# Kernel tuning notes

Hardware: AMD Instinct MI355X
Metric: run time of the kernel (lower is better)

Reference implementation:

```python
import jax, jax.numpy as jnp
import numpy as np

B, TENC, LIS = 32, 2048, 512
HID, EMB, CLS = 512, 256, 64
KEY, VAL, TDEC = 128, 128, 65


def setup_inputs() -> dict:
    key = jax.random.key(0)
    ks = jax.random.split(key, 32)
    s = 0.02
    p = lambda i, shape: jax.random.normal(ks[i], shape, jnp.float32) * s
    return {
        "listener_output": jax.random.normal(ks[0], (B, TENC, LIS), jnp.float32),
        "outputs_length": jax.random.randint(ks[1], (B,), TENC // 2, TENC + 1, jnp.int32),
        "padded_targets": jax.random.randint(ks[2], (B, TDEC), 0, CLS, jnp.int32),
        "teacher_forcing": 1,
        "embed_table": p(3, (CLS, EMB)),
        "W_ih1": p(4, (4 * HID, EMB + VAL)), "W_hh1": p(5, (4 * HID, HID)),
        "b_ih1": p(6, (4 * HID,)), "b_hh1": p(7, (4 * HID,)),
        "W_ih2": p(8, (4 * HID, HID)), "W_hh2": p(9, (4 * HID, HID)),
        "b_ih2": p(10, (4 * HID,)), "b_hh2": p(11, (4 * HID,)),
        "W_s": p(12, (KEY, HID)), "b_s": p(13, (KEY,)),
        "W_h": p(14, (KEY, LIS)), "b_h": p(15, (KEY,)),
        "W_v": p(16, (VAL, LIS)), "b_v": p(17, (VAL,)),
        "W_c": p(18, (CLS, HID + VAL)), "b_c": p(19, (CLS,)),
        "h1_0": p(20, (B, HID)), "c1_0": p(21, (B, HID)),
        "h2_0": p(22, (B, HID)), "c2_0": p(23, (B, HID)),
    }


def _lstm_cell(x, h, c, Wih, Whh, bih, bhh):
    # torch LSTMCell gate order: input, forget, cell, output
    g = x @ Wih.T + bih + h @ Whh.T + bhh
    i, f, gg, o = jnp.split(g, 4, axis=-1)
    c = jax.nn.sigmoid(f) * c + jax.nn.sigmoid(i) * jnp.tanh(gg)
    h = jax.nn.sigmoid(o) * jnp.tanh(c)
    return h, c


def _speller(listener_output, outputs_length, padded_targets, teacher_forcing,
             embed_table, W_ih1, W_hh1, b_ih1, b_hh1, W_ih2, W_hh2, b_ih2, b_hh2,
             W_s, b_s, W_h, b_h, W_v, b_v, W_c, b_c, h1_0, c1_0, h2_0, c2_0):
    Bv, Tenc, _ = listener_output.shape
    timestep = padded_targets.shape[1] - 1
    # time-validity mask; row 0 is left unmasked, matching the original loops (i != 0)
    valid = jnp.arange(Tenc)[None, :] < outputs_length[:, None]          # [B, Tenc]
    row0 = (jnp.arange(Bv) == 0)[:, None]
    mask = jnp.where(row0, True, valid).astype(listener_output.dtype)    # [B, Tenc]
    # key/value projections are step-invariant: hoist out of the loop (same math)
    key_enc = listener_output @ W_h.T + b_h                              # [B, Tenc, KEY]
    value = (listener_output @ W_v.T + b_v) * mask[:, :, None]           # [B, Tenc, VAL]
    tf = jnp.asarray(teacher_forcing, jnp.float32)
    tf_key = jax.random.key(1)
    samp_key = jax.random.key(2)

    def step(carry, i):
        h1, c1, h2, c2, context, preds = carry
        # teacher-forcing coin (np.random.random() < teacher_forcing)
        coin = jax.random.uniform(jax.random.fold_in(tf_key, i)) < tf
        tok = jnp.where(coin, padded_targets[:, jnp.maximum(i - 1, 0)], preds)
        x = jnp.concatenate([embed_table[tok], context], axis=1)
        nh1, nc1 = _lstm_cell(x, h1, c1, W_ih1, W_hh1, b_ih1, b_hh1)
        nh2, nc2 = _lstm_cell(nh1, h2, c2, W_ih2, W_hh2, b_ih2, b_hh2)
        first = i == 0   # step 0 uses the learned initial states, no RNN update
        h1 = jnp.where(first, h1, nh1); c1 = jnp.where(first, c1, nc1)
        h2 = jnp.where(first, h2, nh2); c2 = jnp.where(first, c2, nc2)
        query = h2 @ W_s.T + b_s                                         # [B, KEY]
        energy = jnp.einsum('bk,btk->bt', query, key_enc)                # [B, Tenc]
        att = jax.nn.softmax(energy, axis=1) * mask
        att = att / jnp.maximum(att.sum(axis=1, keepdims=True), 1e-12)   # F.normalize p=1
        context = jnp.einsum('bt,btv->bv', att, value)                   # [B, VAL]
        logits = jnp.concatenate([h2, context], axis=1) @ W_c.T + b_c    # [B, CLS]
        preds = jax.random.categorical(jax.random.fold_in(samp_key, i), logits).astype(jnp.int32)
        return (h1, c1, h2, c2, context, preds), (logits, preds, att)

    init = (h1_0, c1_0, h2_0, c2_0,
            jnp.zeros((Bv, W_v.shape[0]), listener_output.dtype),
            jnp.zeros((Bv,), jnp.int32))
    _, (logits, preds, atts) = jax.lax.scan(step, init, jnp.arange(timestep))
    # logits: [T, B, CLS] (the per-step probs list), preds -> [B, T], atts: [T, B, Tenc]
    return logits, preds.T, atts


def reference(listener_output, outputs_length, padded_targets, teacher_forcing,
              embed_table, W_ih1, W_hh1, b_ih1, b_hh1, W_ih2, W_hh2, b_ih2, b_hh2,
              W_s, b_s, W_h, b_h, W_v, b_v, W_c, b_c, h1_0, c1_0, h2_0, c2_0):
    return _speller(listener_output, outputs_length, padded_targets, teacher_forcing,
                    embed_table, W_ih1, W_hh1, b_ih1, b_hh1, W_ih2, W_hh2, b_ih2, b_hh2,
                    W_s, b_s, W_h, b_h, W_v, b_v, W_c, b_c, h1_0, c1_0, h2_0, c2_0)
```

## Files before the change

kernel.cpp:

```cpp
#include <hip/hip_runtime.h>
#include <stdint.h>
#include <stddef.h>


struct BarCtr { unsigned v; unsigned pad[31]; };

struct P {
  const float* listener; const int* outlen; const int* ptgt;
  const float* embed;
  const float *W_ih1, *W_hh1, *b_ih1, *b_hh1;
  const float *W_ih2, *W_hh2, *b_ih2, *b_hh2;
  const float *W_s, *b_s, *W_h, *b_h, *W_v, *b_v, *W_c, *b_c;
  const float *h1_0, *c1_0, *h2_0, *c2_0;
  float* keyT;
  float* value;
  float* WT1;
  float* WT2;
  float* h1;
  float* c1;
  float* h2;
  float* c2;
  float* wbuf;
  float* ctxnum;
  float* Ssum;
  BarCtr* bar;
  float* out;
};

__device__ __forceinline__ float sigf(float x) { return 1.0f / (1.0f + expf(-x)); }

__device__ __forceinline__ float gload(const float* p) {
  return __hip_atomic_load(p, __ATOMIC_RELAXED, __HIP_MEMORY_SCOPE_AGENT);
}
__device__ __forceinline__ void gstore(float* p, float v) {
  __hip_atomic_store(p, v, __ATOMIC_RELAXED, __HIP_MEMORY_SCOPE_AGENT);
}
__device__ __forceinline__ void gadd(float* p, float v) {
  __hip_atomic_fetch_add(p, v, __ATOMIC_RELAXED, __HIP_MEMORY_SCOPE_AGENT);
}

__device__ __forceinline__ void tf2x32(uint32_t k0, uint32_t k1,
                                       uint32_t x0, uint32_t x1,
                                       uint32_t& o0, uint32_t& o1) {
  uint32_t k2 = k0 ^ k1 ^ 0x1BD11BDAu;
#define TFR(r) { x0 += x1; x1 = (x1 << (r)) | (x1 >> (32 - (r))); x1 ^= x0; }
  x0 += k0; x1 += k1;
  TFR(13) TFR(15) TFR(26) TFR(6)   x0 += k1; x1 += k2 + 1u;
  TFR(17) TFR(29) TFR(16) TFR(24)  x0 += k2; x1 += k0 + 2u;
  TFR(13) TFR(15) TFR(26) TFR(6)   x0 += k0; x1 += k1 + 3u;
  TFR(17) TFR(29) TFR(16) TFR(24)  x0 += k1; x1 += k2 + 4u;
  TFR(13) TFR(15) TFR(26) TFR(6)   x0 += k2; x1 += k0 + 5u;
#undef TFR
  o0 = x0; o1 = x1;
}

__device__ __forceinline__ float gumbel_f(uint32_t bits) {
  float f = __uint_as_float((bits >> 9) | 0x3f800000u) - 1.0f;
  float u = (f == 0.0f) ? 1.17549435e-38f : f;
  return -logf(-logf(u));
}

__device__ __forceinline__ void gbar(BarCtr* bar, int blk, unsigned round) {
  __syncthreads();
  if (threadIdx.x == 0) {
    __hip_atomic_fetch_add(&bar[blk & 7].v, 1u, __ATOMIC_RELAXED, __HIP_MEMORY_SCOPE_AGENT);
    const unsigned tgt = round * 256u;
    for (;;) {
      unsigned s = 0;
#pragma unroll
      for (int c = 0; c < 8; ++c)
        s += __hip_atomic_load(&bar[c].v, __ATOMIC_RELAXED, __HIP_MEMORY_SCOPE_AGENT);
      if (s >= tgt) break;
      __builtin_amdgcn_s_sleep(1);
    }
    asm volatile("" ::: "memory");
  }
  __syncthreads();
}

__global__ void __launch_bounds__(256) k_init(P p) {
  int idx = blockIdx.x * 256 + threadIdx.x;
  p.h1[idx] = p.h1_0[idx];
  p.c1[idx] = p.c1_0[idx];
  p.h2[idx] = p.h2_0[idx];
  p.c2[idx] = p.c2_0[idx];
  if (idx < 8192) p.ctxnum[idx] = 0.0f;
  if (idx < 64)   p.Ssum[idx]   = 0.0f;
  if (idx < 8)    p.bar[idx].v  = 0u;
}

__global__ void __launch_bounds__(256) k_proj(P p) {
  const int blk = blockIdx.x, tid = threadIdx.x;
  const int b = blk >> 7, tb = blk & 127, t0 = tb * 16;
  __shared__ float lst[16 * 512];
  const float* src = p.listener + ((size_t)b * 2048 + t0) * 512;
  for (int n = 0; n < 32; ++n) {
    int idx = n * 256 + tid;
    lst[idx] = src[idx];
  }
  __syncthreads();
  const int c = tid;
  const float* wr = (c < 128) ? (p.W_h + c * 512) : (p.W_v + (c - 128) * 512);
  const float bias = (c < 128) ? p.b_h[c] : p.b_v[c - 128];
  float acc[16];
#pragma unroll
  for (int r = 0; r < 16; ++r) acc[r] = 0.0f;
  for (int k4 = 0; k4 < 128; ++k4) {
    float4 w4 = ((const float4*)wr)[k4];
#pragma unroll
    for (int r = 0; r < 16; ++r) {
      float4 x4 = ((const float4*)(lst + r * 512))[k4];
      acc[r] = fmaf(w4.x, x4.x, fmaf(w4.y, x4.y, fmaf(w4.z, x4.z, fmaf(w4.w, x4.w, acc[r]))));
    }
  }
  if (c < 128) {
#pragma unroll
    for (int r = 0; r < 16; ++r)
      p.keyT[((size_t)b * 128 + c) * 2048 + t0 + r] = acc[r] + bias;
  } else {
#pragma unroll
    for (int r = 0; r < 16; ++r)
      p.value[((size_t)b * 2048 + t0 + r) * 128 + (c - 128)] = acc[r] + bias;
  }
}

__global__ void __launch_bounds__(256) k_tw(P p) {
  __shared__ float t[64 * 65];
  const int blk = blockIdx.x, tid = threadIdx.x;
  const float *Wa, *Wb; float* dst; int kt, ct, ka, sA, sB;
  if (blk < 512) { kt = blk >> 5; ct = blk & 31; Wa = p.W_ih2; sA = 512; Wb = p.W_hh2; sB = 512; ka = 512; dst = p.WT2; }
  else { int b2 = blk - 512; kt = b2 >> 5; ct = b2 & 31; Wa = p.W_ih1; sA = 384; Wb = p.W_hh1; sB = 512; ka = 384; dst = p.WT1; }
  for (int n = 0; n < 4; ++n) {
    int fid = n * 256 + tid;
    int cl = fid >> 4, k4 = (fid & 15) * 4;
    int grow = ((cl >> 4) * 512) + ct * 16 + (cl & 15);
    int k = kt * 64 + k4;
    float4 v = (k < ka) ? *(const float4*)&Wa[(size_t)grow * sA + k]
                        : *(const float4*)&Wb[(size_t)grow * sB + (k - ka)];
    t[cl * 65 + k4 + 0] = v.x; t[cl * 65 + k4 + 1] = v.y;
    t[cl * 65 + k4 + 2] = v.z; t[cl * 65 + k4 + 3] = v.w;
  }
  __syncthreads();
  for (int n = 0; n < 4; ++n) {
    int fid = n * 256 + tid;
    int kl = fid >> 4, c4 = (fid & 15) * 4;
    int k = kt * 64 + kl;
    float4 o;
    o.x = t[(c4 + 0) * 65 + kl]; o.y = t[(c4 + 1) * 65 + kl];
    o.z = t[(c4 + 2) * 65 + kl]; o.w = t[(c4 + 3) * 65 + kl];
    *(float4*)&dst[(size_t)k * 2048 + ct * 64 + c4] = o;
  }
}

__device__ void do_finalize(const P& p, int step, int b, int tid, float* sf) {
  const int c = tid;
  const int par = step & 1;
  const float* h2p  = p.h2 + par * 16384 + b * 512;
  const float* ctxp = p.ctxnum + par * 4096 + b * 128;
  const float invS = 1.0f / fmaxf(gload(&p.Ssum[par * 32 + b]), 1e-12f);
#pragma unroll
  for (int n = 0; n < 10; ++n) {
    int idx = n * 64 + c;
    float v = (idx < 512) ? gload(&h2p[idx]) : gload(&ctxp[idx - 512]) * invS;
    sf[idx] = v;
  }
  asm volatile("s_waitcnt vmcnt(0) lgkmcnt(0)" ::: "memory");
  __builtin_amdgcn_wave_barrier();
  const float* wr = p.W_c + c * 640;
  float a0 = 0.f, a1 = 0.f, a2 = 0.f, a3 = 0.f;
#pragma unroll 8
  for (int k4 = 0; k4 < 160; ++k4) {
    float4 w4 = ((const float4*)wr)[k4];
    float4 x4 = ((const float4*)sf)[k4];
    a0 = fmaf(w4.x, x4.x, a0); a1 = fmaf(w4.y, x4.y, a1);
    a2 = fmaf(w4.z, x4.z, a2); a3 = fmaf(w4.w, x4.w, a3);
  }
  float lg = p.b_c[c] + ((a0 + a1) + (a2 + a3));
  p.out[(size_t)(step * 32 + b) * 64 + c] = lg;
  uint32_t n0, n1, r0, r1;
  tf2x32(0u, 2u, 0u, (uint32_t)step, n0, n1);
  tf2x32(n0, n1, 0u, (uint32_t)(b * 64 + c), r0, r1);
  float z = gumbel_f(r0 ^ r1) + lg;
  int ix = c;
  for (int off = 32; off; off >>= 1) {
    float zz = __shfl_xor(z, off, 64); int ii = __shfl_xor(ix, off, 64);
    if (zz > z || (zz == z && ii < ix)) { z = zz; ix = ii; }
  }
  if (c == 0) p.out[131072 + b * 64 + step] = (float)ix;
}

__device__ void phase_g1(const P& p, int i, float* xT, float* sg, float* sfin, int blk, int tid) {
  const int par = i & 1, q1 = par ^ 1;
  const int bg = blk >> 5, rg = blk & 31;
  if (tid < 256) {
    int flat = blk * 256 + tid;
    int b = flat >> 11, t = flat & 2047;
    float s = fmaxf(gload(&p.Ssum[q1 * 32 + b]), 1e-12f);
    p.out[133120 + (size_t)((i - 1) * 32 + b) * 2048 + t] = gload(&p.wbuf[b * 2048 + t]) / s;
  }
  {
    int b4 = tid & 3, kb = (tid >> 2) << 2;
    if (kb < 896) {
      int b = bg * 4 + b4;
      float v0, v1, v2, v3;
      if (kb < 256) {
        int tok = p.ptgt[b * 65 + (i - 1)];
        const float* e = p.embed + tok * 256 + kb;
        v0 = e[0]; v1 = e[1]; v2 = e[2]; v3 = e[3];
      } else if (kb < 384) {
        float invS = 1.0f / fmaxf(gload(&p.Ssum[q1 * 32 + b]), 1e-12f);
        const float* cx = p.ctxnum + q1 * 4096 + b * 128 + (kb - 256);
        v0 = gload(cx + 0) * invS; v1 = gload(cx + 1) * invS;
        v2 = gload(cx + 2) * invS; v3 = gload(cx + 3) * invS;
      } else {
        const float* h = p.h1 + q1 * 16384 + b * 512 + (kb - 384);
        v0 = gload(h + 0); v1 = gload(h + 1); v2 = gload(h + 2); v3 = gload(h + 3);
      }
      xT[(kb + 0) * 4 + b4] = v0; xT[(kb + 1) * 4 + b4] = v1;
      xT[(kb + 2) * 4 + b4] = v2; xT[(kb + 3) * 4 + b4] = v3;
    }
  }
  if (tid < 256) {
    int lr = tid & 63;
    int grow = (lr >> 4) * 512 + rg * 16 + (lr & 15);
    sg[tid] = p.b_ih1[grow] + p.b_hh1[grow];
  }
  __syncthreads();
  {
    int w = tid >> 6, lane = tid & 63;
    const float* wp = p.WT1 + (size_t)(w * 56) * 2048 + rg * 64 + lane;
    const float4* xp = (const float4*)(xT + (w * 56) * 4);
    float a0 = 0.f, a1 = 0.f, a2 = 0.f, a3 = 0.f;
#pragma unroll 8
    for (int k = 0; k < 56; ++k) {
      float wv = wp[(size_t)k * 2048];
      float4 x4 = xp[k];
      a0 = fmaf(wv, x4.x, a0); a1 = fmaf(wv, x4.y, a1);
      a2 = fmaf(wv, x4.z, a2); a3 = fmaf(wv, x4.w, a3);
    }
    atomicAdd(&sg[lane], a0);        atomicAdd(&sg[64 + lane], a1);
    atomicAdd(&sg[128 + lane], a2);  atomicAdd(&sg[192 + lane], a3);
  }
  __syncthreads();
  if (tid < 64) {
    int bb = tid >> 4, jl = tid & 15;
    int b = bg * 4 + bb, j = rg * 16 + jl;
    float gi = sg[bb * 64 + jl];
    float gf = sg[bb * 64 + 16 + jl];
    float gg = sg[bb * 64 + 32 + jl];
    float go = sg[bb * 64 + 48 + jl];
    float cp = p.c1[q1 * 16384 + b * 512 + j];
    float c  = sigf(gf) * cp + sigf(gi) * tanhf(gg);
    gstore(&p.h1[par * 16384 + b * 512 + j], sigf(go) * tanhf(c));
    p.c1[par * 16384 + b * 512 + j] = c;
  }
  if (blk < 32 && tid < 64) do_finalize(p, i - 1, blk, tid, sfin);
}

__device__ void phase_g2(const P& p, int i, float* xT, float* sg, int blk, int tid) {
  const int par = i & 1, q1 = par ^ 1;
  const int bg = blk >> 5, rg = blk & 31;
  if (blk < 4) gstore(&p.ctxnum[q1 * 4096 + blk * 1024 + tid], 0.0f);
  if (blk == 4 && tid < 32) gstore(&p.Ssum[q1 * 32 + tid], 0.0f);
  {
    int b4 = tid & 3, kb = (tid >> 2) << 2;
    int b = bg * 4 + b4;
    const float* h = (kb < 512) ? (p.h1 + par * 16384 + b * 512 + kb)
                                : (p.h2 + q1 * 16384 + b * 512 + (kb - 512));
    float v0 = gload(h + 0), v1 = gload(h + 1), v2 = gload(h + 2), v3 = gload(h + 3);
    xT[(kb + 0) * 4 + b4] = v0; xT[(kb + 1) * 4 + b4] = v1;
    xT[(kb + 2) * 4 + b4] = v2; xT[(kb + 3) * 4 + b4] = v3;
  }
  if (tid < 256) {
    int lr = tid & 63;
    int grow = (lr >> 4) * 512 + rg * 16 + (lr & 15);
    sg[tid] = p.b_ih2[grow] + p.b_hh2[grow];
  }
  __syncthreads();
  {
    int w = tid >> 6, lane = tid & 63;
    const float* wp = p.WT2 + (size_t)(w * 64) * 2048 + rg * 64 + lane;
    const float4* xp = (const float4*)(xT + (w * 64) * 4);
    float a0 = 0.f, a1 = 0.f, a2 = 0.f, a3 = 0.f;
#pragma unroll 8
    for (int k = 0; k < 64; ++k) {
      float wv = wp[(size_t)k * 2048];
      float4 x4 = xp[k];
      a0 = fmaf(wv, x4.x, a0); a1 = fmaf(wv, x4.y, a1);
      a2 = fmaf(wv, x4.z, a2); a3 = fmaf(wv, x4.w, a3);
    }
    atomicAdd(&sg[lane], a0);        atomicAdd(&sg[64 + lane], a1);
    atomicAdd(&sg[128 + lane], a2);  atomicAdd(&sg[192 + lane], a3);
  }
  __syncthreads();
  if (tid < 64) {
    int bb = tid >> 4, jl = tid & 15;
    int b = bg * 4 + bb, j = rg * 16 + jl;
    float gi = sg[bb * 64 + jl];
    float gf = sg[bb * 64 + 16 + jl];
    float gg = sg[bb * 64 + 32 + jl];
    float go = sg[bb * 64 + 48 + jl];
    float cp = p.c2[q1 * 16384 + b * 512 + j];
    float c  = sigf(gf) * cp + sigf(gi) * tanhf(gg);
    gstore(&p.h2[par * 16384 + b * 512 + j], sigf(go) * tanhf(c));
    p.c2[par * 16384 + b * 512 + j] = c;
  }
}

__device__ __forceinline__ void phase_att(const P& p, int i, float* smem, const float* kslice,
                                          const float va[32], int blk, int tid) {
  const int par = i & 1;
  const int b = blk >> 3;
  float* sh2 = smem;
  float* sq  = smem + 512;
  float* sqp = smem + 640;
  float* se  = smem + 1152;
  float* sw  = smem + 2176;
  float* swr = smem + 2432;
  float* sc  = smem + 2440;
  const float* h2p = p.h2 + par * 16384 + b * 512;
  if (tid < 512) sh2[tid] = gload(&h2p[tid]);
  __syncthreads();
  if (tid < 512) {
    int col = tid & 127, qh = tid >> 7;
    const float* wr = p.W_s + col * 512 + qh * 128;
    const float4* h4p = (const float4*)(sh2 + qh * 128);
    float a0 = 0.f, a1 = 0.f, a2 = 0.f, a3 = 0.f;
#pragma unroll
    for (int j4 = 0; j4 < 32; ++j4) {
      float4 w4 = ((const float4*)wr)[j4], h4 = h4p[j4];
      a0 = fmaf(w4.x, h4.x, a0); a1 = fmaf(w4.y, h4.y, a1);
      a2 = fmaf(w4.z, h4.z, a2); a3 = fmaf(w4.w, h4.w, a3);
    }
    sqp[qh * 128 + col] = (a0 + a1) + (a2 + a3);
  }
  __syncthreads();
  if (tid < 128) sq[tid] = p.b_s[tid] + sqp[tid] + sqp[128 + tid] + sqp[256 + tid] + sqp[384 + tid];
  __syncthreads();
  {
    int tt = tid & 255, kq = tid >> 8;
    const float* kc = kslice + tt;
    const int kb = kq * 32;
    float e0 = 0.f, e1 = 0.f, e2 = 0.f, e3 = 0.f;
#pragma unroll 8
    for (int k = 0; k < 32; k += 4) {
      e0 = fmaf(kc[(kb + k + 0) * 256], sq[kb + k + 0], e0);
      e1 = fmaf(kc[(kb + k + 1) * 256], sq[kb + k + 1], e1);
      e2 = fmaf(kc[(kb + k + 2) * 256], sq[kb + k + 2], e2);
      e3 = fmaf(kc[(kb + k + 3) * 256], sq[kb + k + 3], e3);
    }
    se[kq * 256 + tt] = (e0 + e1) + (e2 + e3);
  }
  __syncthreads();
  if (tid < 256) {
    const int ch = blk & 7, t0 = ch * 256;
    int t = t0 + tid;
    float e = se[tid] + se[256 + tid] + se[512 + tid] + se[768 + tid];
    const int len = p.outlen[b];
    bool msk = (b == 0) || (t < len);
    float wv = msk ? expf(e) : 0.0f;
    gstore(&p.wbuf[b * 2048 + t], wv);
    sw[tid] = wv;
    float s = wv;
    for (int off = 32; off; off >>= 1) s += __shfl_xor(s, off, 64);
    if ((tid & 63) == 0) swr[tid >> 6] = s;
  }
  __syncthreads();
  if (tid == 0) gadd(&p.Ssum[par * 32 + b], swr[0] + swr[1] + swr[2] + swr[3]);
  {
    int v = tid & 127, tp = tid >> 7;
    float c0 = 0.f, c1v = 0.f;
#pragma unroll
    for (int tt2 = 0; tt2 < 32; tt2 += 2) {
      c0  = fmaf(sw[tp * 32 + tt2],     va[tt2],     c0);
      c1v = fmaf(sw[tp * 32 + tt2 + 1], va[tt2 + 1], c1v);
    }
    sc[tp * 128 + v] = c0 + c1v;
  }
  __syncthreads();
  if (tid < 128) {
    float s = 0.f;
#pragma unroll
    for (int tp = 0; tp < 8; ++tp) s += sc[tp * 128 + tid];
    gadd(&p.ctxnum[par * 4096 + b * 128 + tid], s);
  }
}

__global__ void __launch_bounds__(1024, 4) k_loop(P p) {
  __shared__ __align__(16) float kslice[128 * 256];
  __shared__ __align__(16) float work[4096 + 256 + 640];
  float* xT   = work;
  float* sg   = work + 4096;
  float* sfin = work + 4352;
  const int blk = blockIdx.x, tid = threadIdx.x;
  const int b_att = blk >> 3, ch = blk & 7, t0 = ch * 256;
  {
    const float* ksrc = p.keyT + (size_t)b_att * 262144 + t0;
    for (int n = 0; n < 32; ++n) {
      int idx = n * 1024 + tid;
      int k = idx >> 8, tt = idx & 255;
      kslice[k * 256 + tt] = ksrc[(size_t)k * 2048 + tt];
    }
  }
  float va[32];
  {
    int v = tid & 127, tp = tid >> 7;
    const float* vb = p.value + ((size_t)(b_att * 2048 + t0 + tp * 32)) * 128 + v;
#pragma unroll
    for (int tt2 = 0; tt2 < 32; ++tt2) va[tt2] = vb[(size_t)tt2 * 128];
  }
  __syncthreads();
  unsigned nb = 0;
  phase_att(p, 0, work, kslice, va, blk, tid);
  for (int i = 1; i < 64; ++i) {
    gbar(p.bar, blk, ++nb);
    phase_g1(p, i, xT, sg, sfin, blk, tid);
    gbar(p.bar, blk, ++nb);
    phase_g2(p, i, xT, sg, blk, tid);
    gbar(p.bar, blk, ++nb);
    phase_att(p, i, work, kslice, va, blk, tid);
  }
  gbar(p.bar, blk, ++nb);
  if (tid < 256) {
    int flat = blk * 256 + tid;
    int b = flat >> 11, t = flat & 2047;
    float s = fmaxf(gload(&p.Ssum[1 * 32 + b]), 1e-12f);
    p.out[133120 + (size_t)(63 * 32 + b) * 2048 + t] = gload(&p.wbuf[b * 2048 + t]) / s;
  }
  if (blk < 32 && tid < 64) do_finalize(p, 63, blk, tid, sfin);
}

extern "C" void kernel_launch(void* const* d_in, const int* in_sizes, int n_in,
                              void* d_out, int out_size, void* d_ws, size_t ws_size,
                              hipStream_t stream) {
  P p;
  p.listener = (const float*)d_in[0];
  p.outlen   = (const int*)d_in[1];
  p.ptgt     = (const int*)d_in[2];
  p.embed = (const float*)d_in[4];
  p.W_ih1 = (const float*)d_in[5];  p.W_hh1 = (const float*)d_in[6];
  p.b_ih1 = (const float*)d_in[7];  p.b_hh1 = (const float*)d_in[8];
  p.W_ih2 = (const float*)d_in[9];  p.W_hh2 = (const float*)d_in[10];
  p.b_ih2 = (const float*)d_in[11]; p.b_hh2 = (const float*)d_in[12];
  p.W_s = (const float*)d_in[13]; p.b_s = (const float*)d_in[14];
  p.W_h = (const float*)d_in[15]; p.b_h = (const float*)d_in[16];
  p.W_v = (const float*)d_in[17]; p.b_v = (const float*)d_in[18];
  p.W_c = (const float*)d_in[19]; p.b_c = (const float*)d_in[20];
  p.h1_0 = (const float*)d_in[21]; p.c1_0 = (const float*)d_in[22];
  p.h2_0 = (const float*)d_in[23]; p.c2_0 = (const float*)d_in[24];

  char* w = (char*)d_ws;
  p.keyT   = (float*)w; w += (size_t)32 * 128 * 2048 * 4;
  p.value  = (float*)w; w += (size_t)32 * 2048 * 128 * 4;
  p.WT1    = (float*)w; w += (size_t)896 * 2048 * 4;
  p.WT2    = (float*)w; w += (size_t)1024 * 2048 * 4;
  p.h1  = (float*)w; w += 2 * 32 * 512 * 4;
  p.c1  = (float*)w; w += 2 * 32 * 512 * 4;
  p.h2  = (float*)w; w += 2 * 32 * 512 * 4;
  p.c2  = (float*)w; w += 2 * 32 * 512 * 4;
  p.wbuf   = (float*)w; w += 32 * 2048 * 4;
  p.ctxnum = (float*)w; w += 2 * 32 * 128 * 4;
  p.Ssum   = (float*)w; w += 2 * 32 * 4;
  p.bar    = (BarCtr*)w; w += 8 * sizeof(BarCtr);
  p.out = (float*)d_out;

  k_init<<<64, 256, 0, stream>>>(p);
  k_proj<<<4096, 256, 0, stream>>>(p);
  k_tw<<<960, 256, 0, stream>>>(p);
  k_loop<<<256, 1024, 0, stream>>>(p);
}
```

Measured before the change: 6.134 ms.

## Replace global atomic barrier with per-group flag barriers and localize work ownership

```diff
diff --git a/kernel.cpp b/kernel.cpp
--- a/kernel.cpp
+++ b/kernel.cpp
@@ -3,7 +3,7 @@
 #include <stddef.h>
 
 
-struct BarCtr { unsigned v; unsigned pad[31]; };
+struct BarGrp { unsigned v[32]; };
 
 struct P {
   const float* listener; const int* outlen; const int* ptgt;
@@ -23,7 +23,7 @@
   float* wbuf;
   float* ctxnum;
   float* Ssum;
-  BarCtr* bar;
+  BarGrp* bar;
   float* out;
 };
 
@@ -60,17 +60,16 @@
   return -logf(-logf(u));
 }
 
-__device__ __forceinline__ void gbar(BarCtr* bar, int blk, unsigned round) {
-  __syncthreads();
-  if (threadIdx.x == 0) {
-    __hip_atomic_fetch_add(&bar[blk & 7].v, 1u, __ATOMIC_RELAXED, __HIP_MEMORY_SCOPE_AGENT);
-    const unsigned tgt = round * 256u;
+__device__ __forceinline__ void gbar(BarGrp* bar, int blk, unsigned round) {
+  __syncthreads();
+  unsigned* sl = bar[blk >> 5].v;
+  if (threadIdx.x == 0)
+    __hip_atomic_store(&sl[blk & 31], round, __ATOMIC_RELEASE, __HIP_MEMORY_SCOPE_AGENT);
+  if (threadIdx.x < 64) {
     for (;;) {
-      unsigned s = 0;
-#pragma unroll
-      for (int c = 0; c < 8; ++c)
-        s += __hip_atomic_load(&bar[c].v, __ATOMIC_RELAXED, __HIP_MEMORY_SCOPE_AGENT);
-      if (s >= tgt) break;
+      unsigned v = __hip_atomic_load(&sl[threadIdx.x & 31], __ATOMIC_RELAXED,
+                                     __HIP_MEMORY_SCOPE_AGENT);
+      if (__all((int)(v >= round))) break;
       __builtin_amdgcn_s_sleep(1);
     }
     asm volatile("" ::: "memory");
@@ -86,7 +85,7 @@
   p.c2[idx] = p.c2_0[idx];
   if (idx < 8192) p.ctxnum[idx] = 0.0f;
   if (idx < 64)   p.Ssum[idx]   = 0.0f;
-  if (idx < 8)    p.bar[idx].v  = 0u;
+  if (idx < 256)  ((unsigned*)p.bar)[idx] = 0u;
 }
 
 __global__ void __launch_bounds__(256) k_proj(P p) {
@@ -254,14 +253,16 @@
     gstore(&p.h1[par * 16384 + b * 512 + j], sigf(go) * tanhf(c));
     p.c1[par * 16384 + b * 512 + j] = c;
   }
-  if (blk < 32 && tid < 64) do_finalize(p, i - 1, blk, tid, sfin);
+  if (rg < 4 && tid < 64) do_finalize(p, i - 1, bg * 4 + rg, tid, sfin);
 }
 
 __device__ void phase_g2(const P& p, int i, float* xT, float* sg, int blk, int tid) {
   const int par = i & 1, q1 = par ^ 1;
   const int bg = blk >> 5, rg = blk & 31;
-  if (blk < 4) gstore(&p.ctxnum[q1 * 4096 + blk * 1024 + tid], 0.0f);
-  if (blk == 4 && tid < 32) gstore(&p.Ssum[q1 * 32 + tid], 0.0f);
+  if (rg == 0) {
+    if (tid < 512) gstore(&p.ctxnum[q1 * 4096 + bg * 512 + tid], 0.0f);
+    else if (tid < 516) gstore(&p.Ssum[q1 * 32 + bg * 4 + (tid - 512)], 0.0f);
+  }
   {
     int b4 = tid & 3, kb = (tid >> 2) << 2;
     int b = bg * 4 + b4;
@@ -427,7 +428,7 @@
     float s = fmaxf(gload(&p.Ssum[1 * 32 + b]), 1e-12f);
     p.out[133120 + (size_t)(63 * 32 + b) * 2048 + t] = gload(&p.wbuf[b * 2048 + t]) / s;
   }
-  if (blk < 32 && tid < 64) do_finalize(p, 63, blk, tid, sfin);
+  if ((blk & 31) < 4 && tid < 64) do_finalize(p, 63, (blk >> 5) * 4 + (blk & 31), tid, sfin);
 }
 
 extern "C" void kernel_launch(void* const* d_in, const int* in_sizes, int n_in,
@@ -461,7 +462,7 @@
   p.wbuf   = (float*)w; w += 32 * 2048 * 4;
   p.ctxnum = (float*)w; w += 2 * 32 * 128 * 4;
   p.Ssum   = (float*)w; w += 2 * 32 * 4;
-  p.bar    = (BarCtr*)w; w += 8 * sizeof(BarCtr);
+  p.bar    = (BarGrp*)w; w += 8 * sizeof(BarGrp);
   p.out = (float*)d_out;
 
   k_init<<<64, 256, 0, stream>>>(p);
```

After: 6.388 ms. 1.04x slower.
